# Optimization experiments

Hardware: AMD Instinct MI355X
Metric: run time of the kernel (lower is better)

## Reference

```python
import jax, jax.numpy as jnp
import numpy as np

EMBED_DIM = 1024
MODULE_DIM = 128
MODULE_COUNT = 128  # must equal MODULE_DIM for the original matmul to be valid
N_TOKENS = 16384


def setup_inputs() -> dict:
    key = jax.random.key(0)
    ks = jax.random.split(key, 9)
    s_e = 1.0 / np.sqrt(EMBED_DIM)
    s_d = 1.0 / np.sqrt(MODULE_DIM)
    return {
        "h0": jax.random.normal(ks[0], (N_TOKENS, EMBED_DIM), dtype=jnp.float32),
        "we0_w": jax.random.uniform(ks[1], (MODULE_DIM, EMBED_DIM), minval=-s_e, maxval=s_e, dtype=jnp.float32),
        "we0_b": jax.random.uniform(ks[2], (MODULE_DIM,), minval=-s_e, maxval=s_e, dtype=jnp.float32),
        "ws_w": jax.random.uniform(ks[3], (MODULE_COUNT, MODULE_DIM), minval=-s_d, maxval=s_d, dtype=jnp.float32),
        "ws_b": jax.random.uniform(ks[4], (MODULE_COUNT,), minval=-s_d, maxval=s_d, dtype=jnp.float32),
        "wm_w": jax.random.uniform(ks[5], (MODULE_COUNT, MODULE_DIM, MODULE_DIM), minval=-s_d, maxval=s_d, dtype=jnp.float32),
        "wm_b": jax.random.uniform(ks[6], (MODULE_COUNT, MODULE_DIM), minval=-s_d, maxval=s_d, dtype=jnp.float32),
        "we1_w": jax.random.uniform(ks[7], (EMBED_DIM, MODULE_DIM), minval=-s_d, maxval=s_d, dtype=jnp.float32),
        "we1_b": jax.random.uniform(ks[8], (EMBED_DIM,), minval=-s_d, maxval=s_d, dtype=jnp.float32),
    }


def reference(h0, we0_w, we0_b, ws_w, ws_b, wm_w, wm_b, we1_w, we1_b):
    # h0: [N, E]
    enc = h0 @ we0_w.T + we0_b                                   # [N, D]
    # stacked expert linears: acts[m, n, k] = relu(sum_d enc[n,d] * wm_w[m,k,d] + wm_b[m,k])
    acts = jax.nn.relu(jnp.einsum('nd,mkd->mnk', enc, wm_w) + wm_b[:, None, :])  # [M, N, D]
    # gating logits [N, M]; NOTE: softmax over dim 0 (the batch axis), faithful to original
    gate = jax.nn.softmax(enc @ ws_w.T + ws_b, axis=0)           # [N, M]
    # original: matmul(acts.transpose(0,1) [N,M,D], gate[...,None] [N,M,1]) with D == M
    # mixed[n, i] = sum_j acts[i, n, j] * gate[n, j]
    mixed = jnp.einsum('inj,nj->ni', acts, gate)                 # [N, M] (== [N, D])
    decoded = mixed @ we1_w.T + we1_b                            # [N, E]
    return jax.nn.relu(decoded + h0)
```

## Files before the change

### kernel.cpp

```cpp
#include <hip/hip_runtime.h>


#define N_TOK   16384
#define EMB     1024
#define MDIM    128

typedef __attribute__((ext_vector_type(8))) short   short8;
typedef __attribute__((ext_vector_type(4))) float   f32x4;
typedef __attribute__((ext_vector_type(4))) float   fv4;
typedef __attribute__((ext_vector_type(4))) unsigned short us4;

static __device__ __forceinline__ unsigned short f2bf(float f) {
    union { float f; unsigned u; } v; v.f = f;
    unsigned r = v.u + 0x7FFFu + ((v.u >> 16) & 1u);
    return (unsigned short)(r >> 16);
}
static __device__ __forceinline__ float bf2f_lo(unsigned u) {
    union { unsigned u; float f; } v; v.u = u << 16; return v.f;
}
static __device__ __forceinline__ float bf2f_hi(unsigned u) {
    union { unsigned u; float f; } v; v.u = u & 0xffff0000u; return v.f;
}

__global__ void k_convert_all(const float* __restrict__ wm_w,
                              const float* __restrict__ we0_w,
                              const float* __restrict__ we1_w,
                              const float* __restrict__ ws_w,
                              unsigned* __restrict__ wmf8,
                              unsigned short* __restrict__ bf16dst) {
    const int N = 524288 + 36864;
    for (int i = blockIdx.x * blockDim.x + threadIdx.x; i < N;
         i += gridDim.x * blockDim.x) {
        if (i < 524288) {
            fv4 v = *(const fv4*)(wm_w + (size_t)i * 4);
            int pk = __builtin_amdgcn_cvt_pk_fp8_f32(v.x, v.y, 0, false);
            pk = __builtin_amdgcn_cvt_pk_fp8_f32(v.z, v.w, pk, true);
            wmf8[i] = (unsigned)pk;
        } else {
            int j = i - 524288;
            const float* src;
            if (j < 32768)      src = we0_w + (size_t)j * 4;
            else if (j < 65536) src = we1_w + (size_t)(j - 32768) * 4;
            else                src = ws_w  + (size_t)(j - 65536) * 4;
            fv4 v = *(const fv4*)src;
            us4 o;
            o.x = f2bf(v.x); o.y = f2bf(v.y); o.z = f2bf(v.z); o.w = f2bf(v.w);
            *(us4*)(bf16dst + (size_t)j * 4) = o;
        }
    }
}


__global__ __launch_bounds__(256) void k_enc(const float* __restrict__ h0,
                                             const unsigned short* __restrict__ we0b,
                                             const unsigned short* __restrict__ wsb,
                                             const float* __restrict__ we0_bias,
                                             const float* __restrict__ ws_bias,
                                             unsigned char* __restrict__ encF8,
                                             float* __restrict__ logT) {
    __shared__ unsigned short Wt[128 * 128];
    __shared__ unsigned short Ht[32 * 128];
    __shared__ unsigned short Et[32 * 128];

    const int tid = threadIdx.x;
    const int lane = tid & 63, w = tid >> 6;
    const int c = lane & 15, g = lane >> 4;
    const int wd = w >> 1, wt = w & 1;
    const int t0 = blockIdx.x * 32;

    f32x4 acc[4] = {};
    for (int ks = 0; ks < 8; ++ks) {
        #pragma unroll
        for (int it = 0; it < 8; ++it) {
            int m = it * 256 + tid;
            int row = m >> 4, gc = m & 15;
            short8 v = *(const short8*)(we0b + row * 1024 + ks * 128 + gc * 8);
            *(short8*)&Wt[row * 128 + ((gc ^ (row & 7)) * 8)] = v;
        }
        #pragma unroll
        for (int it = 0; it < 2; ++it) {
            int m = it * 256 + tid;
            int row = m >> 4, gc = m & 15;
            const float* hp = h0 + (size_t)(t0 + row) * 1024 + ks * 128 + gc * 8;
            fv4 v0 = *(const fv4*)hp;
            fv4 v1 = *(const fv4*)(hp + 4);
            short8 ov;
            ov[0] = (short)f2bf(v0.x); ov[1] = (short)f2bf(v0.y);
            ov[2] = (short)f2bf(v0.z); ov[3] = (short)f2bf(v0.w);
            ov[4] = (short)f2bf(v1.x); ov[5] = (short)f2bf(v1.y);
            ov[6] = (short)f2bf(v1.z); ov[7] = (short)f2bf(v1.w);
            *(short8*)&Ht[row * 128 + ((gc ^ (row & 7)) * 8)] = ov;
        }
        __syncthreads();
        #pragma unroll
        for (int s = 0; s < 4; ++s) {
            int gk = s * 4 + g;
            int brow = wt * 16 + c;
            short8 b = *(const short8*)&Ht[brow * 128 + ((gk ^ (brow & 7)) * 8)];
            #pragma unroll
            for (int jf = 0; jf < 4; ++jf) {
                int j = wd * 64 + jf * 16 + c;
                short8 a = *(const short8*)&Wt[j * 128 + ((gk ^ (j & 7)) * 8)];
                acc[jf] = __builtin_amdgcn_mfma_f32_16x16x32_bf16(a, b, acc[jf], 0, 0, 0);
            }
        }
        __syncthreads();
    }
    const int tile = blockIdx.x * 2 + wt;
    const int erow = wt * 16 + c;
    #pragma unroll
    for (int f = 0; f < 4; ++f) {
        int d0 = wd * 64 + f * 16 + 4 * g;
        fv4 bi = *(const fv4*)(we0_bias + d0);
        float v0 = acc[f][0] + bi.x, v1 = acc[f][1] + bi.y;
        float v2 = acc[f][2] + bi.z, v3 = acc[f][3] + bi.w;
        int pk = __builtin_amdgcn_cvt_pk_fp8_f32(v0, v1, 0, false);
        pk = __builtin_amdgcn_cvt_pk_fp8_f32(v2, v3, pk, true);
        int s = wd * 2 + (f >> 1);
        int chunk = (f & 1) * 2 + (g >> 1);
        int e = (g & 1) * 4;
        *(unsigned*)(encF8 + (size_t)tile * 2048 + (chunk * 16 + c) * 32 + s * 8 + e) = (unsigned)pk;
        us4 o;
        o.x = f2bf(v0); o.y = f2bf(v1); o.z = f2bf(v2); o.w = f2bf(v3);
        int cg = d0 >> 3, off = d0 & 7;
        *(us4*)&Et[erow * 128 + ((cg ^ (erow & 7)) * 8) + off] = o;
    }
    __syncthreads();

    short8 al[4][4];
    #pragma unroll
    for (int jf = 0; jf < 4; ++jf)
        #pragma unroll
        for (int s = 0; s < 4; ++s)
            al[jf][s] = *(const short8*)(wsb + (wd * 64 + jf * 16 + c) * 128 + s * 32 + g * 8);
    short8 bl[4];
    #pragma unroll
    for (int s = 0; s < 4; ++s) {
        int cg2 = s * 4 + g;
        bl[s] = *(const short8*)&Et[erow * 128 + ((cg2 ^ (erow & 7)) * 8)];
    }
    f32x4 acc2[4] = {};
    #pragma unroll
    for (int s = 0; s < 4; ++s)
        #pragma unroll
        for (int jf = 0; jf < 4; ++jf)
            acc2[jf] = __builtin_amdgcn_mfma_f32_16x16x32_bf16(al[jf][s], bl[s], acc2[jf], 0, 0, 0);
    const int tokc = t0 + wt * 16 + c;
    #pragma unroll
    for (int jf = 0; jf < 4; ++jf) {
        int m0 = wd * 64 + jf * 16 + 4 * g;
        fv4 bs = *(const fv4*)(ws_bias + m0);
        logT[(size_t)(m0 + 0) * N_TOK + tokc] = acc2[jf][0] + bs.x;
        logT[(size_t)(m0 + 1) * N_TOK + tokc] = acc2[jf][1] + bs.y;
        logT[(size_t)(m0 + 2) * N_TOK + tokc] = acc2[jf][2] + bs.z;
        logT[(size_t)(m0 + 3) * N_TOK + tokc] = acc2[jf][3] + bs.w;
    }
}

__global__ __launch_bounds__(1024) void k_softmax0(const float* __restrict__ logT,
                                                   unsigned short* __restrict__ gateT) {
    __shared__ float red[32];
    const int m = blockIdx.x;
    const int tid = threadIdx.x;
    const int lane = tid & 63, wv = tid >> 6;
    const float* row = logT + (size_t)m * N_TOK;

    fv4 v[4];
    float vmax = -3.0e38f;
    #pragma unroll
    for (int it = 0; it < 4; ++it) {
        v[it] = *(const fv4*)(row + it * 4096 + tid * 4);
        vmax = fmaxf(vmax, fmaxf(fmaxf(v[it].x, v[it].y), fmaxf(v[it].z, v[it].w)));
    }
    #pragma unroll
    for (int o = 32; o > 0; o >>= 1) vmax = fmaxf(vmax, __shfl_xor(vmax, o));
    if (lane == 0) red[wv] = vmax;
    __syncthreads();
    float bmax = -3.0e38f;
    #pragma unroll
    for (int k = 0; k < 16; ++k) bmax = fmaxf(bmax, red[k]);

    float s = 0.f;
    #pragma unroll
    for (int it = 0; it < 4; ++it) {
        v[it].x = __expf(v[it].x - bmax); v[it].y = __expf(v[it].y - bmax);
        v[it].z = __expf(v[it].z - bmax); v[it].w = __expf(v[it].w - bmax);
        s += v[it].x + v[it].y + v[it].z + v[it].w;
    }
    #pragma unroll
    for (int o = 32; o > 0; o >>= 1) s += __shfl_xor(s, o);
    if (lane == 0) red[16 + wv] = s;
    __syncthreads();
    float bs = 0.f;
    #pragma unroll
    for (int k = 0; k < 16; ++k) bs += red[16 + k];
    const float inv = 1.f / bs;

    const int q  = m >> 5;
    const int w8 = ((m >> 4) & 1) * 4 + (m & 3);
    const int gl = ((m & 15) >> 2) * 16;
    #pragma unroll
    for (int it = 0; it < 4; ++it) {
        int t = it * 4096 + tid * 4;
        float pv[4] = { v[it].x * inv, v[it].y * inv, v[it].z * inv, v[it].w * inv };
        #pragma unroll
        for (int k = 0; k < 4; ++k) {
            int tok = t + k;
            gateT[(size_t)(tok >> 4) * 2048 + q * 512 + (gl + (tok & 15)) * 8 + w8] = f2bf(pv[k]);
        }
    }
}

__global__ __launch_bounds__(256)
__attribute__((amdgpu_waves_per_eu(3, 3)))
void k_mix(const unsigned char* __restrict__ wmf8,
           const unsigned char* __restrict__ encF8,
           const unsigned short* __restrict__ gateT,
           const float* __restrict__ wm_bias,
           unsigned short* __restrict__ mixT) {
    const int bid = blockIdx.x;
    const int i = bid & 127, part = bid >> 7;
    const int tid = threadIdx.x;
    const int lane = tid & 63, w = tid >> 6;
    const int c = lane & 15, g = lane >> 4;

    const unsigned char* wmi = wmf8 + (size_t)i * 16384;
    uint2 a[8][4];
    #pragma unroll
    for (int jf = 0; jf < 8; ++jf)
        #pragma unroll
        for (int s = 0; s < 4; ++s) {
            a[jf][s] = *(const uint2*)(wmi + (jf * 16 + c) * 128 + s * 32 + g * 8);
            asm volatile("" : "+v"(a[jf][s]));
        }
    f32x4 bias4[8];
    #pragma unroll
    for (int f = 0; f < 8; ++f) {
        bias4[f] = *(const f32x4*)(wm_bias + i * 128 + f * 16 + 4 * g);
        asm volatile("" : "+v"(bias4[f]));
    }

    const int start = part * 42 + (part < 4 ? part : 4);
    const int cnt = 42 + (part < 4 ? 1 : 0);
    const int si = i >> 5, ch = (i & 31) >> 3, ei = i & 7;

    const unsigned char* encB = encF8 + (size_t)(start * 4 + w) * 2048 + lane * 32;
    const unsigned* gateB = (const unsigned*)(gateT + (size_t)(start * 4 + w) * 2048) + lane * 4;
    unsigned short* mixB = mixT + (size_t)(start * 4 + w) * 2048 + si * 512 + (ch * 16 + lane) * 8 + ei;

    uint4 q0 = *(const uint4*)(encB);
    uint4 q1 = *(const uint4*)(encB + 16);

    #pragma unroll 1
    for (int t = 0; t < cnt; ++t) {
        const unsigned* gp = gateB + (size_t)t * 4096;
        uint4 G0 = *(const uint4*)(gp);
        uint4 G1 = *(const uint4*)(gp + 256);
        uint4 G2 = *(const uint4*)(gp + 512);
        uint4 G3 = *(const uint4*)(gp + 768);

        long b0 = __builtin_bit_cast(long, (uint2){q0.x, q0.y});
        long b1 = __builtin_bit_cast(long, (uint2){q0.z, q0.w});
        long b2 = __builtin_bit_cast(long, (uint2){q1.x, q1.y});
        long b3 = __builtin_bit_cast(long, (uint2){q1.z, q1.w});

        __builtin_amdgcn_s_setprio(1);
        f32x4 acc[8];
        #pragma unroll
        for (int jf = 0; jf < 8; ++jf)
            acc[jf] = __builtin_amdgcn_mfma_f32_16x16x32_fp8_fp8(
                __builtin_bit_cast(long, a[jf][0]), b0, bias4[jf], 0, 0, 0);
        #pragma unroll
        for (int jf = 0; jf < 8; ++jf)
            acc[jf] = __builtin_amdgcn_mfma_f32_16x16x32_fp8_fp8(
                __builtin_bit_cast(long, a[jf][1]), b1, acc[jf], 0, 0, 0);
        #pragma unroll
        for (int jf = 0; jf < 8; ++jf)
            acc[jf] = __builtin_amdgcn_mfma_f32_16x16x32_fp8_fp8(
                __builtin_bit_cast(long, a[jf][2]), b2, acc[jf], 0, 0, 0);
        #pragma unroll
        for (int jf = 0; jf < 8; ++jf)
            acc[jf] = __builtin_amdgcn_mfma_f32_16x16x32_fp8_fp8(
                __builtin_bit_cast(long, a[jf][3]), b3, acc[jf], 0, 0, 0);
        __builtin_amdgcn_s_setprio(0);

        {
            const int tn = (t + 1 < cnt) ? t + 1 : t;
            const unsigned char* ebn = encB + (size_t)tn * 8192;
            q0 = *(const uint4*)(ebn);
            q1 = *(const uint4*)(ebn + 16);
        }

        float p0 = 0.f, p1 = 0.f, p2 = 0.f, p3 = 0.f;
        #define EPI(F, GA, GB) {                                        \
            p0 += fmaxf(acc[F][0], 0.f) * bf2f_lo(GA);                  \
            p1 += fmaxf(acc[F][1], 0.f) * bf2f_hi(GA);                  \
            p2 += fmaxf(acc[F][2], 0.f) * bf2f_lo(GB);                  \
            p3 += fmaxf(acc[F][3], 0.f) * bf2f_hi(GB);                  \
        }
        EPI(0, G0.x, G0.y) EPI(1, G0.z, G0.w)
        EPI(2, G1.x, G1.y) EPI(3, G1.z, G1.w)
        EPI(4, G2.x, G2.y) EPI(5, G2.z, G2.w)
        EPI(6, G3.x, G3.y) EPI(7, G3.z, G3.w)
        #undef EPI
        float p = (p0 + p1) + (p2 + p3);
        p += __shfl_xor(p, 16);
        p += __shfl_xor(p, 32);
        if (lane < 16) *(mixB + (size_t)t * 8192) = f2bf(p);
    }
}

__global__ __launch_bounds__(256)
__attribute__((amdgpu_waves_per_eu(2, 2)))
void k_dec(const unsigned short* __restrict__ we1b,
           const unsigned short* __restrict__ mixT,
           const float* __restrict__ we1_bias,
           const float* __restrict__ h0,
           float* __restrict__ out) {
    const int bid = blockIdx.x;
    const int eb = bid & 7, tg = bid >> 3;
    const int e0 = eb * 128;
    const int tid = threadIdx.x;
    const int lane = tid & 63, w = tid >> 6;
    const int c = lane & 15, g = lane >> 4;

    short8 a[8][4];
    #pragma unroll
    for (int jf = 0; jf < 8; ++jf)
        #pragma unroll
        for (int s = 0; s < 4; ++s) {
            a[jf][s] = *(const short8*)(we1b + (size_t)(e0 + jf * 16 + c) * 128 + s * 32 + g * 8);
            asm volatile("" : "+v"(a[jf][s]));
        }
    fv4 bi[8];
    #pragma unroll
    for (int f = 0; f < 8; ++f)
        bi[f] = *(const fv4*)(we1_bias + e0 + f * 16 + 4 * g);

    #pragma unroll 1
    for (int t = 0; t < 4; ++t) {
        const int tokr = tg * 256 + t * 64 + w * 16 + c;
        const int tile = tg * 16 + t * 4 + w;
        fv4 h[8];
        #pragma unroll
        for (int f = 0; f < 8; ++f)
            h[f] = *(const fv4*)(h0 + (size_t)tokr * 1024 + e0 + f * 16 + 4 * g);
        const unsigned short* mp = mixT + (size_t)tile * 2048 + lane * 8;
        short8 b[4];
        #pragma unroll
        for (int s = 0; s < 4; ++s)
            b[s] = *(const short8*)(mp + s * 512);

        f32x4 acc[8] = {};
        #pragma unroll
        for (int s = 0; s < 4; ++s)
            #pragma unroll
            for (int jf = 0; jf < 8; ++jf)
                acc[jf] = __builtin_amdgcn_mfma_f32_16x16x32_bf16(a[jf][s], b[s], acc[jf], 0, 0, 0);

        #pragma unroll
        for (int f = 0; f < 8; ++f) {
            fv4 o;
            o.x = fmaxf(acc[f][0] + bi[f].x + h[f].x, 0.f);
            o.y = fmaxf(acc[f][1] + bi[f].y + h[f].y, 0.f);
            o.z = fmaxf(acc[f][2] + bi[f].z + h[f].z, 0.f);
            o.w = fmaxf(acc[f][3] + bi[f].w + h[f].w, 0.f);
            *(fv4*)(out + (size_t)tokr * 1024 + e0 + f * 16 + 4 * g) = o;
        }
    }
}

extern "C" void kernel_launch(void* const* d_in, const int* in_sizes, int n_in,
                              void* d_out, int out_size, void* d_ws, size_t ws_size,
                              hipStream_t stream) {
    const float* h0    = (const float*)d_in[0];
    const float* we0_w = (const float*)d_in[1];
    const float* we0_b = (const float*)d_in[2];
    const float* ws_w  = (const float*)d_in[3];
    const float* ws_b  = (const float*)d_in[4];
    const float* wm_w  = (const float*)d_in[5];
    const float* wm_b  = (const float*)d_in[6];
    const float* we1_w = (const float*)d_in[7];
    const float* we1_b = (const float*)d_in[8];
    float* out = (float*)d_out;

    unsigned*       wmf8  = (unsigned*)d_ws;
    unsigned short* we0b  = (unsigned short*)(wmf8 + 524288);
    unsigned short* we1b  = we0b + 131072;
    unsigned short* wsb   = we1b + 131072;
    unsigned char*  encF8 = (unsigned char*)(wsb + 16384);
    float*          logT  = (float*)(encF8 + 2097152);
    unsigned short* gateT = (unsigned short*)(logT + 2097152);
    unsigned short* mixT  = gateT + 2097152;

    k_convert_all<<<640, 256, 0, stream>>>(wm_w, we0_w, we1_w, ws_w, wmf8, we0b);
    k_enc<<<512, 256, 0, stream>>>(h0, we0b, wsb, we0_b, ws_b, encF8, logT);
    k_softmax0<<<128, 1024, 0, stream>>>(logT, gateT);
    k_mix<<<768, 256, 0, stream>>>((const unsigned char*)wmf8, encF8, gateT, wm_b, mixT);
    k_dec<<<512, 256, 0, stream>>>(we1b, mixT, we1_b, h0, out);
}
```

Baseline: 158.2 us.

## Stage expert weight panel in LDS for k_mix and raise occupancy

The conversion kernel now writes each expert's fp8 weights in an MFMA-fragment-friendly layout. k_mix copies that 16 KB panel and the bias into shared memory once per block and reads A fragments from LDS each iteration, instead of holding them all in registers. Freeing those registers lets the kernel target 4 waves per EU instead of 3. The grid becomes 1024 blocks with 8 equal token parts per expert. In exchange, every MFMA now depends on an LDS read inside the inner loop, which adds LDS traffic and latency.

New measurement: 249.8 us. +57.9%, slower.

```diff
diff --git a/kernel.cpp b/kernel.cpp
--- a/kernel.cpp
+++ b/kernel.cpp
@@ -26,7 +26,7 @@
                               const float* __restrict__ we0_w,
                               const float* __restrict__ we1_w,
                               const float* __restrict__ ws_w,
-                              unsigned* __restrict__ wmf8,
+                              unsigned char* __restrict__ wmf8,
                               unsigned short* __restrict__ bf16dst) {
     const int N = 524288 + 36864;
     for (int i = blockIdx.x * blockDim.x + threadIdx.x; i < N;
@@ -35,7 +35,13 @@
             fv4 v = *(const fv4*)(wm_w + (size_t)i * 4);
             int pk = __builtin_amdgcn_cvt_pk_fp8_f32(v.x, v.y, 0, false);
             pk = __builtin_amdgcn_cvt_pk_fp8_f32(v.z, v.w, pk, true);
-            wmf8[i] = (unsigned)pk;
+            int mi = i >> 12;
+            int r  = i & 4095;
+            int j  = r >> 5;
+            int k0 = (r & 31) * 4;
+            int off = mi * 16384 + (((j >> 4) * 4 + (k0 >> 5)) << 9)
+                    + (((((k0 >> 3) & 3) << 4) + (j & 15)) << 3) + (k0 & 7);
+            *(unsigned*)(wmf8 + off) = (unsigned)pk;
         } else {
             int j = i - 524288;
             const float* src;
@@ -212,47 +218,43 @@
 }
 
 __global__ __launch_bounds__(256)
-__attribute__((amdgpu_waves_per_eu(3, 3)))
+__attribute__((amdgpu_waves_per_eu(4, 4)))
 void k_mix(const unsigned char* __restrict__ wmf8,
            const unsigned char* __restrict__ encF8,
            const unsigned short* __restrict__ gateT,
            const float* __restrict__ wm_bias,
            unsigned short* __restrict__ mixT) {
+    __shared__ unsigned char pan[16384];
+    __shared__ float biasl[128];
+
     const int bid = blockIdx.x;
-    const int i = bid & 127, part = bid >> 7;
+    const int i = bid >> 3, part = bid & 7;
     const int tid = threadIdx.x;
     const int lane = tid & 63, w = tid >> 6;
     const int c = lane & 15, g = lane >> 4;
-
-    const unsigned char* wmi = wmf8 + (size_t)i * 16384;
-    uint2 a[8][4];
-    #pragma unroll
-    for (int jf = 0; jf < 8; ++jf)
-        #pragma unroll
-        for (int s = 0; s < 4; ++s) {
-            a[jf][s] = *(const uint2*)(wmi + (jf * 16 + c) * 128 + s * 32 + g * 8);
-            asm volatile("" : "+v"(a[jf][s]));
-        }
-    f32x4 bias4[8];
-    #pragma unroll
-    for (int f = 0; f < 8; ++f) {
-        bias4[f] = *(const f32x4*)(wm_bias + i * 128 + f * 16 + 4 * g);
-        asm volatile("" : "+v"(bias4[f]));
-    }
-
-    const int start = part * 42 + (part < 4 ? part : 4);
-    const int cnt = 42 + (part < 4 ? 1 : 0);
+    (void)c;
+
+    {
+        const uint4* src = (const uint4*)(wmf8 + (size_t)i * 16384);
+        uint4* dst = (uint4*)pan;
+        #pragma unroll
+        for (int r = 0; r < 4; ++r) dst[r * 256 + tid] = src[r * 256 + tid];
+        if (tid < 32) ((fv4*)biasl)[tid] = *(const fv4*)(wm_bias + i * 128 + tid * 4);
+    }
+    __syncthreads();
+
+    const int start = part * 128;
     const int si = i >> 5, ch = (i & 31) >> 3, ei = i & 7;
 
-    const unsigned char* encB = encF8 + (size_t)(start * 4 + w) * 2048 + lane * 32;
-    const unsigned* gateB = (const unsigned*)(gateT + (size_t)(start * 4 + w) * 2048) + lane * 4;
-    unsigned short* mixB = mixT + (size_t)(start * 4 + w) * 2048 + si * 512 + (ch * 16 + lane) * 8 + ei;
+    const unsigned char* encB = encF8 + (size_t)(start + w) * 2048 + lane * 32;
+    const unsigned* gateB = (const unsigned*)(gateT + (size_t)(start + w) * 2048) + lane * 4;
+    unsigned short* mixB = mixT + (size_t)(start + w) * 2048 + si * 512 + (ch * 16 + lane) * 8 + ei;
 
     uint4 q0 = *(const uint4*)(encB);
     uint4 q1 = *(const uint4*)(encB + 16);
 
     #pragma unroll 1
-    for (int t = 0; t < cnt; ++t) {
+    for (int t = 0; t < 32; ++t) {
         const unsigned* gp = gateB + (size_t)t * 4096;
         uint4 G0 = *(const uint4*)(gp);
         uint4 G1 = *(const uint4*)(gp + 256);
@@ -267,25 +269,30 @@
         __builtin_amdgcn_s_setprio(1);
         f32x4 acc[8];
         #pragma unroll
-        for (int jf = 0; jf < 8; ++jf)
-            acc[jf] = __builtin_amdgcn_mfma_f32_16x16x32_fp8_fp8(
-                __builtin_bit_cast(long, a[jf][0]), b0, bias4[jf], 0, 0, 0);
-        #pragma unroll
-        for (int jf = 0; jf < 8; ++jf)
-            acc[jf] = __builtin_amdgcn_mfma_f32_16x16x32_fp8_fp8(
-                __builtin_bit_cast(long, a[jf][1]), b1, acc[jf], 0, 0, 0);
-        #pragma unroll
-        for (int jf = 0; jf < 8; ++jf)
-            acc[jf] = __builtin_amdgcn_mfma_f32_16x16x32_fp8_fp8(
-                __builtin_bit_cast(long, a[jf][2]), b2, acc[jf], 0, 0, 0);
-        #pragma unroll
-        for (int jf = 0; jf < 8; ++jf)
-            acc[jf] = __builtin_amdgcn_mfma_f32_16x16x32_fp8_fp8(
-                __builtin_bit_cast(long, a[jf][3]), b3, acc[jf], 0, 0, 0);
+        for (int jf = 0; jf < 8; ++jf) {
+            long af = __builtin_bit_cast(long, *(const uint2*)&pan[(jf * 4 + 0) * 512 + lane * 8]);
+            fv4 bv = *(const fv4*)&biasl[jf * 16 + 4 * g];
+            acc[jf] = __builtin_amdgcn_mfma_f32_16x16x32_fp8_fp8(af, b0, *(f32x4*)&bv, 0, 0, 0);
+        }
+        #pragma unroll
+        for (int jf = 0; jf < 8; ++jf) {
+            long af = __builtin_bit_cast(long, *(const uint2*)&pan[(jf * 4 + 1) * 512 + lane * 8]);
+            acc[jf] = __builtin_amdgcn_mfma_f32_16x16x32_fp8_fp8(af, b1, acc[jf], 0, 0, 0);
+        }
+        #pragma unroll
+        for (int jf = 0; jf < 8; ++jf) {
+            long af = __builtin_bit_cast(long, *(const uint2*)&pan[(jf * 4 + 2) * 512 + lane * 8]);
+            acc[jf] = __builtin_amdgcn_mfma_f32_16x16x32_fp8_fp8(af, b2, acc[jf], 0, 0, 0);
+        }
+        #pragma unroll
+        for (int jf = 0; jf < 8; ++jf) {
+            long af = __builtin_bit_cast(long, *(const uint2*)&pan[(jf * 4 + 3) * 512 + lane * 8]);
+            acc[jf] = __builtin_amdgcn_mfma_f32_16x16x32_fp8_fp8(af, b3, acc[jf], 0, 0, 0);
+        }
         __builtin_amdgcn_s_setprio(0);
 
         {
-            const int tn = (t + 1 < cnt) ? t + 1 : t;
+            const int tn = (t + 1 < 32) ? t + 1 : t;
             const unsigned char* ebn = encB + (size_t)tn * 8192;
             q0 = *(const uint4*)(ebn);
             q1 = *(const uint4*)(ebn + 16);
@@ -384,8 +391,8 @@
     const float* we1_b = (const float*)d_in[8];
     float* out = (float*)d_out;
 
-    unsigned*       wmf8  = (unsigned*)d_ws;
-    unsigned short* we0b  = (unsigned short*)(wmf8 + 524288);
+    unsigned char*  wmf8  = (unsigned char*)d_ws;
+    unsigned short* we0b  = (unsigned short*)(wmf8 + 2097152);
     unsigned short* we1b  = we0b + 131072;
     unsigned short* wsb   = we1b + 131072;
     unsigned char*  encF8 = (unsigned char*)(wsb + 16384);
@@ -396,6 +403,6 @@
     k_convert_all<<<640, 256, 0, stream>>>(wm_w, we0_w, we1_w, ws_w, wmf8, we0b);
     k_enc<<<512, 256, 0, stream>>>(h0, we0b, wsb, we0_b, ws_b, encF8, logT);
     k_softmax0<<<128, 1024, 0, stream>>>(logT, gateT);
-    k_mix<<<768, 256, 0, stream>>>((const unsigned char*)wmf8, encF8, gateT, wm_b, mixT);
+    k_mix<<<1024, 256, 0, stream>>>(wmf8, encF8, gateT, wm_b, mixT);
     k_dec<<<512, 256, 0, stream>>>(we1b, mixT, we1_b, h0, out);
 }
```

## Stage decoder weights in swizzled LDS and rebalance k_dec grid to 768 blocks

Applied to the files above, without the earlier changes.

The decoder kernel no longer holds the 128x128 bf16 weight tile in registers. It stages the tile in LDS with an XOR swizzle and reads it per MFMA, which frees VGPRs so waves_per_eu can rise from 2 to 3. The grid grows from 512 to 768 blocks, and token tiles are split unevenly (3 or 2 groups per block) so the 256 CUs are loaded more evenly. The cost is extra LDS reads inside the MFMA loop and a one-time shared-memory fill per block.

Result: slower. 169.9 us (+7.4%).

```diff
diff --git a/kernel.cpp b/kernel.cpp
--- a/kernel.cpp
+++ b/kernel.cpp
@@ -311,12 +311,14 @@
 }
 
 __global__ __launch_bounds__(256)
-__attribute__((amdgpu_waves_per_eu(2, 2)))
+__attribute__((amdgpu_waves_per_eu(3, 3)))
 void k_dec(const unsigned short* __restrict__ we1b,
            const unsigned short* __restrict__ mixT,
            const float* __restrict__ we1_bias,
            const float* __restrict__ h0,
            float* __restrict__ out) {
+    __shared__ unsigned short Pt[128 * 128];
+
     const int bid = blockIdx.x;
     const int eb = bid & 7, tg = bid >> 3;
     const int e0 = eb * 128;
@@ -324,23 +326,27 @@
     const int lane = tid & 63, w = tid >> 6;
     const int c = lane & 15, g = lane >> 4;
 
-    short8 a[8][4];
-    #pragma unroll
-    for (int jf = 0; jf < 8; ++jf)
-        #pragma unroll
-        for (int s = 0; s < 4; ++s) {
-            a[jf][s] = *(const short8*)(we1b + (size_t)(e0 + jf * 16 + c) * 128 + s * 32 + g * 8);
-            asm volatile("" : "+v"(a[jf][s]));
-        }
+    #pragma unroll
+    for (int it = 0; it < 8; ++it) {
+        int m = it * 256 + tid;
+        int row = m >> 4, gc = m & 15;
+        short8 v = *(const short8*)(we1b + (size_t)(e0 + row) * 128 + gc * 8);
+        *(short8*)&Pt[row * 128 + ((gc ^ (row & 7)) * 8)] = v;
+    }
+    __syncthreads();
+
     fv4 bi[8];
     #pragma unroll
     for (int f = 0; f < 8; ++f)
         bi[f] = *(const fv4*)(we1_bias + e0 + f * 16 + 4 * g);
 
+    const int start = tg * 2 + (tg < 64 ? tg : 64);
+    const int cnt = 2 + (tg < 64 ? 1 : 0);
+
     #pragma unroll 1
-    for (int t = 0; t < 4; ++t) {
-        const int tokr = tg * 256 + t * 64 + w * 16 + c;
-        const int tile = tg * 16 + t * 4 + w;
+    for (int t = 0; t < cnt; ++t) {
+        const int tile = (start + t) * 4 + w;
+        const int tokr = tile * 16 + c;
         fv4 h[8];
         #pragma unroll
         for (int f = 0; f < 8; ++f)
@@ -353,10 +359,15 @@
 
         f32x4 acc[8] = {};
         #pragma unroll
-        for (int s = 0; s < 4; ++s)
+        for (int s = 0; s < 4; ++s) {
+            int gk = s * 4 + g;
             #pragma unroll
-            for (int jf = 0; jf < 8; ++jf)
-                acc[jf] = __builtin_amdgcn_mfma_f32_16x16x32_bf16(a[jf][s], b[s], acc[jf], 0, 0, 0);
+            for (int jf = 0; jf < 8; ++jf) {
+                int row = jf * 16 + c;
+                short8 av = *(const short8*)&Pt[row * 128 + ((gk ^ (row & 7)) * 8)];
+                acc[jf] = __builtin_amdgcn_mfma_f32_16x16x32_bf16(av, b[s], acc[jf], 0, 0, 0);
+            }
+        }
 
         #pragma unroll
         for (int f = 0; f < 8; ++f) {
@@ -397,5 +408,5 @@
     k_enc<<<512, 256, 0, stream>>>(h0, we0b, wsb, we0_b, ws_b, encF8, logT);
     k_softmax0<<<128, 1024, 0, stream>>>(logT, gateT);
     k_mix<<<768, 256, 0, stream>>>((const unsigned char*)wmf8, encF8, gateT, wm_b, mixT);
-    k_dec<<<512, 256, 0, stream>>>(we1b, mixT, we1_b, h0, out);
-}
+    k_dec<<<768, 256, 0, stream>>>(we1b, mixT, we1_b, h0, out);
+}
```
